# Performance work log

Measured on AMD Instinct MI355X. Metric: run time of the kernel, lower is better.

Reference implementation:

```python
import jax, jax.numpy as jnp
import numpy as np

N_NODES = 100000
N_EDGES = 3200000
_EPS = 1e-6

# SE3 layout: [tx, ty, tz, qx, qy, qz, qw] (pypose convention)

def _normalize_se3(T):
    t, q = T[..., :3], T[..., 3:7]
    q = q / jnp.linalg.norm(q, axis=-1, keepdims=True)
    return jnp.concatenate([t, q], axis=-1)

def _qmul(q, r):
    qx, qy, qz, qw = q[..., 0], q[..., 1], q[..., 2], q[..., 3]
    rx, ry, rz, rw = r[..., 0], r[..., 1], r[..., 2], r[..., 3]
    x = qw * rx + qx * rw + qy * rz - qz * ry
    y = qw * ry - qx * rz + qy * rw + qz * rx
    z = qw * rz + qx * ry - qy * rx + qz * rw
    w = qw * rw - qx * rx - qy * ry - qz * rz
    return jnp.stack([x, y, z, w], axis=-1)

def _qrot(q, v):
    # rotate vector v by unit quaternion q: v + 2 w (u x v) + 2 u x (u x v)
    u, w = q[..., :3], q[..., 3:4]
    t = 2.0 * jnp.cross(u, v)
    return v + w * t + jnp.cross(u, t)

def _se3_inv(T):
    t, q = T[..., :3], T[..., 3:7]
    qc = q * jnp.asarray([-1.0, -1.0, -1.0, 1.0], dtype=T.dtype)
    ti = -_qrot(qc, t)
    return jnp.concatenate([ti, qc], axis=-1)

def _se3_mul(A, B):
    ta, qa = A[..., :3], A[..., 3:7]
    tb, qb = B[..., :3], B[..., 3:7]
    return jnp.concatenate([ta + _qrot(qa, tb), _qmul(qa, qb)], axis=-1)

def _so3_log(q):
    # quaternion (xyzw) -> axis-angle 3-vector
    v, w = q[..., :3], q[..., 3]
    n = jnp.linalg.norm(v, axis=-1)
    n_safe = jnp.where(n > _EPS, n, 1.0)
    scale = jnp.where(n > _EPS, 2.0 * jnp.arctan2(n, w) / n_safe, 2.0 / jnp.where(jnp.abs(w) > _EPS, w, 1.0))
    return v * scale[..., None]

def _se3_log(T):
    # SE3 -> se3 = [tau(3), phi(3)], tau = Jl(phi)^{-1} t
    t, q = T[..., :3], T[..., 3:7]
    phi = _so3_log(q)
    theta = jnp.linalg.norm(phi, axis=-1)
    small = theta < _EPS
    th = jnp.where(small, 1.0, theta)
    c = jnp.where(small, 1.0 / 12.0, 1.0 / th**2 - (1.0 + jnp.cos(th)) / (2.0 * th * jnp.sin(th)))
    pxt = jnp.cross(phi, t)
    tau = t - 0.5 * pxt + c[..., None] * jnp.cross(phi, pxt)
    return jnp.concatenate([tau, phi], axis=-1)

def setup_inputs() -> dict:
    key = jax.random.key(0)
    k1, k2, k3 = jax.random.split(key, 3)
    nodes = _normalize_se3(jax.random.normal(k1, (N_NODES, 7), dtype=jnp.float32))
    poses = _normalize_se3(jax.random.normal(k2, (N_EDGES, 7), dtype=jnp.float32))
    edges = jax.random.randint(k3, (N_EDGES, 2), 0, N_NODES, dtype=jnp.int64)
    return {"edges": edges, "poses": poses, "nodes": nodes}

def reference(edges, poses, nodes):
    node1 = nodes[edges[..., 0]]  # [E, 7]
    node2 = nodes[edges[..., 1]]  # [E, 7]
    error = _se3_mul(_se3_mul(_se3_inv(poses), node2), _se3_inv(node1))
    return _se3_log(error)  # [E, 6]
```

## Files before the change

### kernel.cpp

```cpp
#include <hip/hip_runtime.h>
#include <math.h>

#define BLOCK 256
#define EPS 1e-6f

struct F3 { float x, y, z; };
struct F4 { float x, y, z, w; };
struct TP { F3 tau; F3 phi; };

__device__ __forceinline__ F3 cross3(F3 a, F3 b) {
    return F3{a.y * b.z - a.z * b.y,
              a.z * b.x - a.x * b.z,
              a.x * b.y - a.y * b.x};
}
__device__ __forceinline__ F3 add3(F3 a, F3 b) { return F3{a.x + b.x, a.y + b.y, a.z + b.z}; }
__device__ __forceinline__ F3 neg3(F3 a) { return F3{-a.x, -a.y, -a.z}; }

__device__ __forceinline__ F3 qrot(F4 q, F3 v) {
    F3 u{q.x, q.y, q.z};
    F3 t = cross3(u, v);
    t.x *= 2.0f; t.y *= 2.0f; t.z *= 2.0f;
    F3 c = cross3(u, t);
    return F3{v.x + q.w * t.x + c.x,
              v.y + q.w * t.y + c.y,
              v.z + q.w * t.z + c.z};
}
__device__ __forceinline__ F4 qmul(F4 q, F4 r) {
    return F4{
        q.w * r.x + q.x * r.w + q.y * r.z - q.z * r.y,
        q.w * r.y - q.x * r.z + q.y * r.w + q.z * r.x,
        q.w * r.z + q.x * r.y - q.y * r.x + q.z * r.w,
        q.w * r.w - q.x * r.x - q.y * r.y - q.z * r.z};
}

__device__ __forceinline__ float fast_atan2(float y, float x) {
    float ax = fabsf(x);
    float hi = fmaxf(ax, y);
    float lo = fminf(ax, y);
    float r  = lo * __builtin_amdgcn_rcpf(hi);
    float r2 = r * r;
    float p = -0.0117212f;
    p = fmaf(p, r2, 0.05265332f);
    p = fmaf(p, r2, -0.11643287f);
    p = fmaf(p, r2, 0.19354346f);
    p = fmaf(p, r2, -0.33262347f);
    p = fmaf(p, r2, 0.99997726f);
    float a = r * p;
    if (y > ax) a = 1.57079632679f - a;
    if (x < 0.0f) a = 3.14159265359f - a;
    return a;
}

__device__ __forceinline__ TP compute_edge(
    F3 tp, F4 qp, F3 t1, F4 q1, F3 t2, F4 q2)
{
    F4 qpc{-qp.x, -qp.y, -qp.z, qp.w};
    F3 tpi = neg3(qrot(qpc, tp));

    F3 tA = add3(tpi, qrot(qpc, t2));
    F4 qA = qmul(qpc, q2);

    F4 q1c{-q1.x, -q1.y, -q1.z, q1.w};
    F3 t1i = neg3(qrot(q1c, t1));

    F3 tE = add3(tA, qrot(qA, t1i));
    F4 qE = qmul(qA, q1c);

    F3 v{qE.x, qE.y, qE.z};
    float w = qE.w;
    float nn = __builtin_amdgcn_sqrtf(v.x * v.x + v.y * v.y + v.z * v.z);
    float scale;
    if (nn > EPS) {
        scale = 2.0f * fast_atan2(nn, w) * __builtin_amdgcn_rcpf(nn);
    } else {
        float w_safe = (fabsf(w) > EPS) ? w : 1.0f;
        scale = 2.0f * __builtin_amdgcn_rcpf(w_safe);
    }
    F3 phi{v.x * scale, v.y * scale, v.z * scale};

    float theta2 = phi.x * phi.x + phi.y * phi.y + phi.z * phi.z;
    float theta = __builtin_amdgcn_sqrtf(theta2);
    bool small = theta < EPS;
    float th = small ? 1.0f : theta;
    float s   = __sinf(th);
    float cth = __cosf(th);
    float c = small ? (1.0f / 12.0f)
                    : (__builtin_amdgcn_rcpf(th * th)
                       - (1.0f + cth) * __builtin_amdgcn_rcpf(2.0f * th * s));
    F3 pxt  = cross3(phi, tE);
    F3 ppxt = cross3(phi, pxt);
    TP r;
    r.tau = F3{tE.x - 0.5f * pxt.x + c * ppxt.x,
               tE.y - 0.5f * pxt.y + c * ppxt.y,
               tE.z - 0.5f * pxt.z + c * ppxt.z};
    r.phi = phi;
    return r;
}

__global__ void __launch_bounds__(BLOCK) repack_nodes_kernel(
    const float* __restrict__ nodes, float* __restrict__ nodes8, int total7)
{
    int idx = blockIdx.x * BLOCK + threadIdx.x;
    int stride = gridDim.x * BLOCK;
    for (; idx < total7; idx += stride) {
        int node = idx / 7;
        int comp = idx - node * 7;
        nodes8[node * 8 + comp] = nodes[idx];
    }
}

__global__ void __launch_bounds__(BLOCK, 4) pose_graph_pair_kernel(
    const int*   __restrict__ edges,
    const float* __restrict__ poses,
    const float* __restrict__ nodes8,
    float*       __restrict__ out,
    int n)
{
    const long long gid = (long long)blockIdx.x * BLOCK + threadIdx.x;
    const long long e0 = gid * 2;
    if (e0 >= n) return;

    if (e0 + 1 < n) {
        const int4 ed = ((const int4*)edges)[gid];

        const float2* pp = (const float2*)(poses + e0 * 7);
        float2 p0 = pp[0], p1 = pp[1], p2 = pp[2], p3 = pp[3];
        float2 p4 = pp[4], p5 = pp[5], p6 = pp[6];

        const float4* nA1 = (const float4*)(nodes8 + ((size_t)ed.x << 3));
        const float4* nA2 = (const float4*)(nodes8 + ((size_t)ed.y << 3));
        const float4* nB1 = (const float4*)(nodes8 + ((size_t)ed.z << 3));
        const float4* nB2 = (const float4*)(nodes8 + ((size_t)ed.w << 3));
        float4 a1 = nA1[0], a1b = nA1[1];
        float4 a2 = nA2[0], a2b = nA2[1];
        float4 b1 = nB1[0], b1b = nB1[1];
        float4 b2 = nB2[0], b2b = nB2[1];

        TP r0 = compute_edge(
            F3{p0.x, p0.y, p1.x}, F4{p1.y, p2.x, p2.y, p3.x},
            F3{a1.x, a1.y, a1.z}, F4{a1.w, a1b.x, a1b.y, a1b.z},
            F3{a2.x, a2.y, a2.z}, F4{a2.w, a2b.x, a2b.y, a2b.z});

        TP r1 = compute_edge(
            F3{p3.y, p4.x, p4.y}, F4{p5.x, p5.y, p6.x, p6.y},
            F3{b1.x, b1.y, b1.z}, F4{b1.w, b1b.x, b1b.y, b1b.z},
            F3{b2.x, b2.y, b2.z}, F4{b2.w, b2b.x, b2b.y, b2b.z});

        float4* od = (float4*)(out + e0 * 6);
        od[0] = float4{r0.tau.x, r0.tau.y, r0.tau.z, r0.phi.x};
        od[1] = float4{r0.phi.y, r0.phi.z, r1.tau.x, r1.tau.y};
        od[2] = float4{r1.tau.z, r1.phi.x, r1.phi.y, r1.phi.z};
    } else {
        const int2 ed = ((const int2*)edges)[e0];
        const float* p = poses + e0 * 7;
        const float4* n1p = (const float4*)(nodes8 + ((size_t)ed.x << 3));
        const float4* n2p = (const float4*)(nodes8 + ((size_t)ed.y << 3));
        float4 a1 = n1p[0], a1b = n1p[1];
        float4 a2 = n2p[0], a2b = n2p[1];
        TP r = compute_edge(
            F3{p[0], p[1], p[2]}, F4{p[3], p[4], p[5], p[6]},
            F3{a1.x, a1.y, a1.z}, F4{a1.w, a1b.x, a1b.y, a1b.z},
            F3{a2.x, a2.y, a2.z}, F4{a2.w, a2b.x, a2b.y, a2b.z});
        float* o = out + e0 * 6;
        o[0] = r.tau.x; o[1] = r.tau.y; o[2] = r.tau.z;
        o[3] = r.phi.x; o[4] = r.phi.y; o[5] = r.phi.z;
    }
}

__global__ void __launch_bounds__(BLOCK) pose_graph_kernel_fallback(
    const int* __restrict__ edges, const float* __restrict__ poses,
    const float* __restrict__ nodes, float* __restrict__ out, int n)
{
    const long long e = (long long)blockIdx.x * BLOCK + threadIdx.x;
    if (e >= n) return;
    const int2 ed = ((const int2*)edges)[e];
    const float* p = poses + e * 7;
    const float* n1p = nodes + (size_t)ed.x * 7;
    const float* n2p = nodes + (size_t)ed.y * 7;
    TP r = compute_edge(
        F3{p[0], p[1], p[2]}, F4{p[3], p[4], p[5], p[6]},
        F3{n1p[0], n1p[1], n1p[2]}, F4{n1p[3], n1p[4], n1p[5], n1p[6]},
        F3{n2p[0], n2p[1], n2p[2]}, F4{n2p[3], n2p[4], n2p[5], n2p[6]});
    float* o = out + e * 6;
    o[0] = r.tau.x; o[1] = r.tau.y; o[2] = r.tau.z;
    o[3] = r.phi.x; o[4] = r.phi.y; o[5] = r.phi.z;
}

extern "C" void kernel_launch(void* const* d_in, const int* in_sizes, int n_in,
                              void* d_out, int out_size, void* d_ws, size_t ws_size,
                              hipStream_t stream) {
    const int* edges = (const int*)d_in[0];
    const float* poses = (const float*)d_in[1];
    const float* nodes = (const float*)d_in[2];
    float* out = (float*)d_out;

    const int n_edges = in_sizes[0] / 2;
    const int n_nodes = in_sizes[2] / 7;

    const size_t ws_needed = (size_t)n_nodes * 8 * sizeof(float);
    if (ws_size >= ws_needed) {
        float* nodes8 = (float*)d_ws;
        const int total7 = n_nodes * 7;
        const int rgrid = (total7 + BLOCK - 1) / BLOCK;
        repack_nodes_kernel<<<rgrid, BLOCK, 0, stream>>>(nodes, nodes8, total7);
        const int n_pairs = (n_edges + 1) / 2;
        const int grid = (n_pairs + BLOCK - 1) / BLOCK;
        pose_graph_pair_kernel<<<grid, BLOCK, 0, stream>>>(edges, poses, nodes8, out, n_edges);
    } else {
        const int grid = (n_edges + BLOCK - 1) / BLOCK;
        pose_graph_kernel_fallback<<<grid, BLOCK, 0, stream>>>(edges, poses, nodes, out, n_edges);
    }
}
```

Baseline: 239.6 us.

## Stage pose loads and output stores through per-wave LDS for coalescing

Replaces the two-edges-per-thread kernel with one edge per thread, where each wave loads its 64 poses with fully coalesced strided reads into shared memory and transposes them to per-thread AoS. Outputs are likewise written to shared memory and then stored as coalesced float2 chunks. The aim is to remove the partially coalesced 28-byte-stride pose loads and 24-byte-stride output stores. In exchange it adds LDS traffic, possible bank conflicts at stride 7 and 6, and half the per-thread ILP compared with the paired version. No barrier is needed because each wave uses only its own slab.

Result: faster. 232.3 us (-3.0%).

```diff
diff --git a/kernel.cpp b/kernel.cpp
--- a/kernel.cpp
+++ b/kernel.cpp
@@ -109,50 +109,62 @@
     }
 }
 
-__global__ void __launch_bounds__(BLOCK, 4) pose_graph_pair_kernel(
+__global__ void __launch_bounds__(BLOCK) pose_graph_kernel(
     const int*   __restrict__ edges,
     const float* __restrict__ poses,
     const float* __restrict__ nodes8,
     float*       __restrict__ out,
     int n)
 {
-    const long long gid = (long long)blockIdx.x * BLOCK + threadIdx.x;
-    const long long e0 = gid * 2;
-    if (e0 >= n) return;
-
-    if (e0 + 1 < n) {
-        const int4 ed = ((const int4*)edges)[gid];
-
-        const float2* pp = (const float2*)(poses + e0 * 7);
-        float2 p0 = pp[0], p1 = pp[1], p2 = pp[2], p3 = pp[3];
-        float2 p4 = pp[4], p5 = pp[5], p6 = pp[6];
-
-        const float4* nA1 = (const float4*)(nodes8 + ((size_t)ed.x << 3));
-        const float4* nA2 = (const float4*)(nodes8 + ((size_t)ed.y << 3));
-        const float4* nB1 = (const float4*)(nodes8 + ((size_t)ed.z << 3));
-        const float4* nB2 = (const float4*)(nodes8 + ((size_t)ed.w << 3));
-        float4 a1 = nA1[0], a1b = nA1[1];
-        float4 a2 = nA2[0], a2b = nA2[1];
-        float4 b1 = nB1[0], b1b = nB1[1];
-        float4 b2 = nB2[0], b2b = nB2[1];
-
-        TP r0 = compute_edge(
-            F3{p0.x, p0.y, p1.x}, F4{p1.y, p2.x, p2.y, p3.x},
+    __shared__ float slab[4 * 448];
+
+    const int tid  = threadIdx.x;
+    const int wave = tid >> 6;
+    const int lane = tid & 63;
+    float* ws = &slab[wave * 448];
+
+    const long long base = (long long)blockIdx.x * BLOCK;
+    const long long e = base + tid;
+    const long long wbase = base + (long long)wave * 64;
+
+    if (base + BLOCK <= n) {
+        const int2 ed = ((const int2*)edges)[e];
+
+        const float* psrc = poses + wbase * 7;
+        float pv[7];
+        #pragma unroll
+        for (int k = 0; k < 7; ++k) pv[k] = psrc[lane + k * 64];
+
+        const float4* n1p = (const float4*)(nodes8 + ((size_t)ed.x << 3));
+        const float4* n2p = (const float4*)(nodes8 + ((size_t)ed.y << 3));
+        float4 a1 = n1p[0], a1b = n1p[1];
+        float4 a2 = n2p[0], a2b = n2p[1];
+
+        #pragma unroll
+        for (int k = 0; k < 7; ++k) ws[lane + k * 64] = pv[k];
+        float p[7];
+        #pragma unroll
+        for (int k = 0; k < 7; ++k) p[k] = ws[lane * 7 + k];
+
+        TP r = compute_edge(
+            F3{p[0], p[1], p[2]}, F4{p[3], p[4], p[5], p[6]},
             F3{a1.x, a1.y, a1.z}, F4{a1.w, a1b.x, a1b.y, a1b.z},
             F3{a2.x, a2.y, a2.z}, F4{a2.w, a2b.x, a2b.y, a2b.z});
 
-        TP r1 = compute_edge(
-            F3{p3.y, p4.x, p4.y}, F4{p5.x, p5.y, p6.x, p6.y},
-            F3{b1.x, b1.y, b1.z}, F4{b1.w, b1b.x, b1b.y, b1b.z},
-            F3{b2.x, b2.y, b2.z}, F4{b2.w, b2b.x, b2b.y, b2b.z});
-
-        float4* od = (float4*)(out + e0 * 6);
-        od[0] = float4{r0.tau.x, r0.tau.y, r0.tau.z, r0.phi.x};
-        od[1] = float4{r0.phi.y, r0.phi.z, r1.tau.x, r1.tau.y};
-        od[2] = float4{r1.tau.z, r1.phi.x, r1.phi.y, r1.phi.z};
-    } else {
-        const int2 ed = ((const int2*)edges)[e0];
-        const float* p = poses + e0 * 7;
+        ws[lane * 6 + 0] = r.tau.x;
+        ws[lane * 6 + 1] = r.tau.y;
+        ws[lane * 6 + 2] = r.tau.z;
+        ws[lane * 6 + 3] = r.phi.x;
+        ws[lane * 6 + 4] = r.phi.y;
+        ws[lane * 6 + 5] = r.phi.z;
+
+        const float2* ov = (const float2*)ws;
+        float2* od = (float2*)(out + wbase * 6);
+        #pragma unroll
+        for (int k = 0; k < 3; ++k) od[lane + k * 64] = ov[lane + k * 64];
+    } else if (e < n) {
+        const int2 ed = ((const int2*)edges)[e];
+        const float* p = poses + e * 7;
         const float4* n1p = (const float4*)(nodes8 + ((size_t)ed.x << 3));
         const float4* n2p = (const float4*)(nodes8 + ((size_t)ed.y << 3));
         float4 a1 = n1p[0], a1b = n1p[1];
@@ -161,7 +173,7 @@
             F3{p[0], p[1], p[2]}, F4{p[3], p[4], p[5], p[6]},
             F3{a1.x, a1.y, a1.z}, F4{a1.w, a1b.x, a1b.y, a1b.z},
             F3{a2.x, a2.y, a2.z}, F4{a2.w, a2b.x, a2b.y, a2b.z});
-        float* o = out + e0 * 6;
+        float* o = out + e * 6;
         o[0] = r.tau.x; o[1] = r.tau.y; o[2] = r.tau.z;
         o[3] = r.phi.x; o[4] = r.phi.y; o[5] = r.phi.z;
     }
@@ -196,6 +208,7 @@
 
     const int n_edges = in_sizes[0] / 2;
     const int n_nodes = in_sizes[2] / 7;
+    const int grid = (n_edges + BLOCK - 1) / BLOCK;
 
     const size_t ws_needed = (size_t)n_nodes * 8 * sizeof(float);
     if (ws_size >= ws_needed) {
@@ -203,11 +216,8 @@
         const int total7 = n_nodes * 7;
         const int rgrid = (total7 + BLOCK - 1) / BLOCK;
         repack_nodes_kernel<<<rgrid, BLOCK, 0, stream>>>(nodes, nodes8, total7);
-        const int n_pairs = (n_edges + 1) / 2;
-        const int grid = (n_pairs + BLOCK - 1) / BLOCK;
-        pose_graph_pair_kernel<<<grid, BLOCK, 0, stream>>>(edges, poses, nodes8, out, n_edges);
+        pose_graph_kernel<<<grid, BLOCK, 0, stream>>>(edges, poses, nodes8, out, n_edges);
     } else {
-        const int grid = (n_edges + BLOCK - 1) / BLOCK;
         pose_graph_kernel_fallback<<<grid, BLOCK, 0, stream>>>(edges, poses, nodes, out, n_edges);
     }
 }
```
